# Kernel tuning notes

Measured on AMD Instinct MI355X. Metric: run time of the kernel, lower is better.

The kernel has to match this reference:

```python
import jax, jax.numpy as jnp
import numpy as np

B, N, K = 16, 2048, 32
DT = 0.01      # leapfrog step size
EPS = 1e-8     # SPD regularization (matches spd_exponential_map default)


def _sym(M):
    return 0.5 * (M + jnp.swapaxes(M, -1, -2))


def _ensure_spd(S, eps=1e-6):
    # Project to SPD cone via eigenvalue clipping: V max(L, eps) V^T
    I = jnp.eye(S.shape[-1], dtype=S.dtype)
    S = _sym(S + eps * I)
    w, v = jnp.linalg.eigh(S)
    w = jnp.clip(w, eps)
    return _sym(jnp.einsum('...ik,...k,...jk->...ij', v, w, v))


def _spd_expmap(Sigma, V, eps=1e-8):
    # exp_Sigma(V) = S^{1/2} exp(S^{-1/2} V S^{-1/2}) S^{1/2}
    I = jnp.eye(Sigma.shape[-1], dtype=Sigma.dtype)
    S = _sym(Sigma) + eps * I
    w, v = jnp.linalg.eigh(S)
    w = jnp.clip(w, eps)
    sq = jnp.sqrt(w)
    S_sqrt = jnp.einsum('...ik,...k,...jk->...ij', v, sq, v)
    S_isqrt = jnp.einsum('...ik,...k,...jk->...ij', v, 1.0 / sq, v)
    W = _sym(S_isqrt @ V @ S_isqrt)
    ww, wv = jnp.linalg.eigh(W)
    ww = jnp.clip(ww, -20.0, 20.0)
    expW = jnp.einsum('...ik,...k,...jk->...ij', wv, jnp.exp(ww), wv)
    return _ensure_spd(S_sqrt @ expW @ S_sqrt, eps)


def _retract_mod2pi(phi, margin=0.01):
    # Wrap axis-angle field into principal ball ||phi|| < pi - margin
    eps = 1e-12
    r_max = jnp.pi - margin
    theta = jnp.linalg.norm(phi, axis=-1, keepdims=True)
    theta_safe = jnp.maximum(theta, eps)
    axis = phi / theta_safe
    two_pi = 2.0 * jnp.pi
    tw = jnp.remainder(theta, two_pi)
    flip = tw > jnp.pi
    t_final = jnp.where(flip, two_pi - tw, tw)
    a_final = jnp.where(flip, -axis, axis)
    t_final = jnp.minimum(t_final, r_max)
    return a_final * t_final


def setup_inputs() -> dict:
    key = jax.random.key(0)
    k1, k2, k3, k4 = jax.random.split(key, 4)
    # Build well-conditioned SPD covariances: Wishart/K + I
    A = jax.random.normal(k1, (B, N, K, K), jnp.float32)
    Sigma = A @ jnp.swapaxes(A, -1, -2) / K + jnp.eye(K, dtype=jnp.float32)
    pi_Sigma = _sym(jax.random.normal(k2, (B, N, K, K), jnp.float32)) * 0.1
    phi = jax.random.normal(k3, (B, N, 3), jnp.float32) * 2.0
    pi_phi = jax.random.normal(k4, (B, N, 3), jnp.float32)
    return {"Sigma": Sigma, "pi_Sigma": pi_Sigma, "phi": phi, "pi_phi": pi_phi}


def reference(Sigma, pi_Sigma, phi, pi_phi):
    # One leapfrog step on the (Sigma, phi) sector of the phase space.
    # Momentum half-step: force from curved geometry dT/dSigma = 2 pi S pi
    grad_T = _sym(2.0 * (pi_Sigma @ Sigma @ pi_Sigma))
    pi_half = pi_Sigma - 0.5 * DT * grad_T
    # Position update via SPD exponential map with Sigma_dot = 2 S pi S
    Sigma_dot = 2.0 * (Sigma @ pi_half @ Sigma)
    Sigma_new = _spd_expmap(Sigma, DT * Sigma_dot, EPS)
    # Gauge field update + mod2pi retraction to principal ball
    phi_new = _retract_mod2pi(phi + DT * pi_phi)
    b, n = Sigma_new.shape[:2]
    return jnp.concatenate([Sigma_new.reshape(b, n, K * K), phi_new], axis=-1)
```

## Files before the change

### kernel.cpp

```cpp
#include <hip/hip_runtime.h>
#include <hip/hip_bf16.h>
#include <math.h>


typedef unsigned int u32;
typedef __attribute__((ext_vector_type(8))) short bf16x8;
typedef __attribute__((ext_vector_type(16))) float f32x16;

#define FPAD 33

union U4 { u32 u[4]; bf16x8 v; };

__device__ __forceinline__ bf16x8 mk8(u32 a, u32 b, u32 c, u32 d) {
    U4 t; t.u[0] = a; t.u[1] = b; t.u[2] = c; t.u[3] = d; return t.v;
}

__device__ __forceinline__ u32 pk2(float x, float y) {
    float2 f2; f2.x = x; f2.y = y;
    __hip_bfloat162 h2 = __float22bfloat162_rn(f2);
    union { __hip_bfloat162 h; u32 u; } c; c.h = h2; return c.u;
}

__device__ __forceinline__ float asfloat(u32 b) {
    union { u32 u; float f; } c; c.u = b; return c.f;
}

__device__ __forceinline__ f32x16 zero16() {
    f32x16 z;
#pragma unroll
    for (int i = 0; i < 16; ++i) z[i] = 0.f;
    return z;
}

struct Frag8 { u32 r[8]; };

__device__ __forceinline__ void swap32(u32& x, u32& y) {
    asm("v_permlane32_swap_b32 %0, %1" : "+v"(x), "+v"(y));
}

__device__ __forceinline__ void xchg(const u32* p, Frag8& B) {
    { u32 x = p[0], y = p[2]; swap32(x, y); B.r[0] = x; B.r[2] = y; }
    { u32 x = p[1], y = p[3]; swap32(x, y); B.r[1] = x; B.r[3] = y; }
    { u32 x = p[4], y = p[6]; swap32(x, y); B.r[4] = x; B.r[6] = y; }
    { u32 x = p[5], y = p[7]; swap32(x, y); B.r[5] = x; B.r[7] = y; }
}

__device__ __forceinline__ void bconv(const f32x16& X, Frag8& B) {
    u32 p[8];
#pragma unroll
    for (int i = 0; i < 8; ++i) p[i] = pk2(X[2*i], X[2*i+1]);
    xchg(p, B);
}

__device__ __forceinline__ void bconv_s(const f32x16& X, float scale, Frag8& B) {
    u32 p[8];
#pragma unroll
    for (int i = 0; i < 8; ++i) p[i] = pk2(X[2*i] * scale, X[2*i+1] * scale);
    xchg(p, B);
}

__device__ __forceinline__ void bconv_split(const f32x16& X, Frag8& Bh, Frag8& Bl) {
    u32 p[8], q[8];
#pragma unroll
    for (int i = 0; i < 8; ++i) {
        const float x = X[2*i], y = X[2*i+1];
        p[i] = pk2(x, y);
        const float lx = x - asfloat(p[i] << 16);
        const float ly = y - asfloat(p[i] & 0xffff0000u);
        q[i] = pk2(lx, ly);
    }
    xchg(p, Bh);
    xchg(q, Bl);
}

__device__ __forceinline__ f32x16 MFMA1(const u32* a, const u32* b, f32x16 acc) {
    return __builtin_amdgcn_mfma_f32_32x32x16_bf16(
        mk8(a[0], a[1], a[2], a[3]), mk8(b[0], b[1], b[2], b[3]), acc, 0, 0, 0);
}

__device__ __forceinline__ f32x16 matmul(const Frag8& A, const Frag8& B, f32x16 acc) {
    __builtin_amdgcn_s_setprio(1);
    acc = MFMA1(A.r,     B.r,     acc);
    acc = MFMA1(A.r + 4, B.r + 4, acc);
    __builtin_amdgcn_s_setprio(0);
    return acc;
}

__global__ __launch_bounds__(256)
void leapfrog_fused(const float* __restrict__ Sg, const float* __restrict__ Pg,
                    const float* __restrict__ phig, const float* __restrict__ piphig,
                    float* __restrict__ out, int total)
{
    __shared__ __align__(16) float symb[4 * 32 * FPAD];

    const int w  = threadIdx.x >> 6;
    const int l  = threadIdx.x & 63;
    const int bn = blockIdx.x * 4 + w;
    if (bn >= total) return;

    float* sy = symb + w * 32 * FPAD;

    const int fr = l & 31;
    const int h  = l >> 5;
    const size_t gbase = (size_t)bn * 1024;

    const float* Srow = Sg + gbase + fr * 32 + h * 8;
    const float* Prow = Pg + gbase + fr * 32 + h * 8;
    const float4 sv[4] = { *(const float4*)(Srow +  0), *(const float4*)(Srow +  4),
                           *(const float4*)(Srow + 16), *(const float4*)(Srow + 20) };
    const float4 pv[4] = { *(const float4*)(Prow +  0), *(const float4*)(Prow +  4),
                           *(const float4*)(Prow + 16), *(const float4*)(Prow + 20) };
    const float phx = phig[3 * bn + 0], phy = phig[3 * bn + 1], phz = phig[3 * bn + 2];
    const float qhx = piphig[3 * bn + 0], qhy = piphig[3 * bn + 1], qhz = piphig[3 * bn + 2];

    Frag8 FS, FSl, FP;
#pragma unroll
    for (int i = 0; i < 4; ++i) {
        const float4 s = sv[i];
        const float4 p = pv[i];
        const u32 ha = pk2(s.x, s.y);
        const u32 hb = pk2(s.z, s.w);
        FS.r[2*i]   = ha;
        FS.r[2*i+1] = hb;
        const float lx = s.x - asfloat(ha << 16);
        const float ly = s.y - asfloat(ha & 0xffff0000u);
        const float lz = s.z - asfloat(hb << 16);
        const float lw = s.w - asfloat(hb & 0xffff0000u);
        FSl.r[2*i]   = pk2(lx, ly);
        FSl.r[2*i+1] = pk2(lz, lw);
        FP.r[2*i]   = pk2(p.x, p.y);
        FP.r[2*i+1] = pk2(p.z, p.w);
    }

    f32x16 If;
#pragma unroll
    for (int i = 0; i < 16; ++i)
        If[i] = (((i & 3) + 8 * (i >> 2) + 4 * h) == fr) ? 1.f : 0.f;

    f32x16 U  = matmul(FS, FP, zero16());
    f32x16 Ut = matmul(FP, FS, zero16());
    Frag8 BU;  bconv(U,  BU);
    Frag8 BUt; bconv(Ut, BUt);
    f32x16 H = matmul(BUt, BU, zero16());

    f32x16 M;
#pragma unroll
    for (int i = 0; i < 16; ++i) M[i] = 0.02f * U[i] - 2e-4f * H[i];

    Frag8 FM; bconv(M, FM);

    f32x16 X = If;
#pragma unroll
    for (int d = 3; d >= 1; --d) {
        Frag8 BX; bconv_s(X, 1.f / (float)d, BX);
        X = matmul(FM, BX, If);
    }

    Frag8 BE, BEl;
    bconv_split(X, BE, BEl);
    f32x16 Y1 = matmul(FS, BE, zero16());
    f32x16 Y2 = matmul(FSl, BE, zero16());
    Y2 = matmul(FS, BEl, Y2);

#pragma unroll
    for (int i = 0; i < 16; ++i) {
        const int r = (i & 3) + 8 * (i >> 2) + 4 * h;
        sy[r * FPAD + fr] = Y1[i] + Y2[i];
    }
    const size_t obase = (size_t)bn * 1027;
#pragma unroll
    for (int k = 0; k < 16; ++k) {
        const int idx = k * 64 + l;
        const int r = idx >> 5, c = idx & 31;
        const float a = sy[r * FPAD + c];
        const float b = sy[c * FPAD + r];
        float v = 0.5f * (a + b);
        if (r == c) v += 1e-8f;
        __builtin_nontemporal_store(v, &out[obase + idx]);
    }

    if (l == 0) {
        const double TWO_PI = 6.283185307179586476925287;
        const double PI_    = 3.141592653589793238462643;
        const double x = (double)phx + 0.01 * (double)qhx;
        const double y = (double)phy + 0.01 * (double)qhy;
        const double z = (double)phz + 0.01 * (double)qhz;
        const double theta = sqrt(x * x + y * y + z * z);
        const double ts = theta > 1e-12 ? theta : 1e-12;
        const double k2 = floor(theta * (1.0 / TWO_PI));
        const double tw = theta - k2 * TWO_PI;
        double t, sgn;
        if (tw > PI_) { t = TWO_PI - tw; sgn = -1.0; }
        else          { t = tw;          sgn = 1.0;  }
        const double rmax = PI_ - 0.01;
        if (t > rmax) t = rmax;
        const double f = sgn * t / ts;
        __builtin_nontemporal_store((float)(x * f), &out[obase + 1024]);
        __builtin_nontemporal_store((float)(y * f), &out[obase + 1025]);
        __builtin_nontemporal_store((float)(z * f), &out[obase + 1026]);
    }
}

extern "C" void kernel_launch(void* const* d_in, const int* in_sizes, int n_in,
                              void* d_out, int out_size, void* d_ws, size_t ws_size,
                              hipStream_t stream)
{
    const float* Sg     = (const float*)d_in[0];
    const float* Pg     = (const float*)d_in[1];
    const float* phig   = (const float*)d_in[2];
    const float* piphig = (const float*)d_in[3];
    float* out = (float*)d_out;

    const int total = in_sizes[0] / 1024;

    leapfrog_fused<<<(total + 3) / 4, 256, 0, stream>>>(Sg, Pg, phig, piphig, out, total);
}
```

Measured before the change: 74.83 us.

## Software-pipeline matrix loads across waves and drop LDS symmetrization

Each wave now handles several matrices in a grid-stride loop, prefetching the next matrix's inputs into registers while computing the current one. The shared-memory transpose used for symmetrization is replaced by computing both S·E and E·S with extra MFMAs and averaging in registers, storing straight to global. The priority hints are also removed. This trades extra MFMA work and register pressure for no LDS round trip and better latency hiding, but cuts the grid size by a factor of four.

Result: slower. 80.87 us (+8.1%).

```diff
diff --git a/kernel.cpp b/kernel.cpp
--- a/kernel.cpp
+++ b/kernel.cpp
@@ -7,7 +7,7 @@
 typedef __attribute__((ext_vector_type(8))) short bf16x8;
 typedef __attribute__((ext_vector_type(16))) float f32x16;
 
-#define FPAD 33
+#define ITERS 4
 
 union U4 { u32 u[4]; bf16x8 v; };
 
@@ -79,45 +79,45 @@
 }
 
 __device__ __forceinline__ f32x16 matmul(const Frag8& A, const Frag8& B, f32x16 acc) {
-    __builtin_amdgcn_s_setprio(1);
     acc = MFMA1(A.r,     B.r,     acc);
     acc = MFMA1(A.r + 4, B.r + 4, acc);
-    __builtin_amdgcn_s_setprio(0);
     return acc;
 }
 
-__global__ __launch_bounds__(256)
-void leapfrog_fused(const float* __restrict__ Sg, const float* __restrict__ Pg,
-                    const float* __restrict__ phig, const float* __restrict__ piphig,
-                    float* __restrict__ out, int total)
-{
-    __shared__ __align__(16) float symb[4 * 32 * FPAD];
-
-    const int w  = threadIdx.x >> 6;
-    const int l  = threadIdx.x & 63;
-    const int bn = blockIdx.x * 4 + w;
-    if (bn >= total) return;
-
-    float* sy = symb + w * 32 * FPAD;
-
-    const int fr = l & 31;
-    const int h  = l >> 5;
+struct InBuf {
+    float4 sv[4], pv[4];
+    float  ph[3], pq[3];
+};
+
+__device__ __forceinline__ void loadm(const float* __restrict__ Sg,
+                                      const float* __restrict__ Pg,
+                                      const float* __restrict__ phig,
+                                      const float* __restrict__ piphig,
+                                      int bn, int fr, int h, InBuf& b)
+{
     const size_t gbase = (size_t)bn * 1024;
-
     const float* Srow = Sg + gbase + fr * 32 + h * 8;
     const float* Prow = Pg + gbase + fr * 32 + h * 8;
-    const float4 sv[4] = { *(const float4*)(Srow +  0), *(const float4*)(Srow +  4),
-                           *(const float4*)(Srow + 16), *(const float4*)(Srow + 20) };
-    const float4 pv[4] = { *(const float4*)(Prow +  0), *(const float4*)(Prow +  4),
-                           *(const float4*)(Prow + 16), *(const float4*)(Prow + 20) };
-    const float phx = phig[3 * bn + 0], phy = phig[3 * bn + 1], phz = phig[3 * bn + 2];
-    const float qhx = piphig[3 * bn + 0], qhy = piphig[3 * bn + 1], qhz = piphig[3 * bn + 2];
-
+    b.sv[0] = *(const float4*)(Srow +  0);
+    b.sv[1] = *(const float4*)(Srow +  4);
+    b.sv[2] = *(const float4*)(Srow + 16);
+    b.sv[3] = *(const float4*)(Srow + 20);
+    b.pv[0] = *(const float4*)(Prow +  0);
+    b.pv[1] = *(const float4*)(Prow +  4);
+    b.pv[2] = *(const float4*)(Prow + 16);
+    b.pv[3] = *(const float4*)(Prow + 20);
+    b.ph[0] = phig[3 * bn + 0]; b.ph[1] = phig[3 * bn + 1]; b.ph[2] = phig[3 * bn + 2];
+    b.pq[0] = piphig[3 * bn + 0]; b.pq[1] = piphig[3 * bn + 1]; b.pq[2] = piphig[3 * bn + 2];
+}
+
+__device__ __forceinline__ void computem(const InBuf& b, float* __restrict__ out,
+                                         int bn, int fr, int h, int l)
+{
     Frag8 FS, FSl, FP;
 #pragma unroll
     for (int i = 0; i < 4; ++i) {
-        const float4 s = sv[i];
-        const float4 p = pv[i];
+        const float4 s = b.sv[i];
+        const float4 p = b.pv[i];
         const u32 ha = pk2(s.x, s.y);
         const u32 hb = pk2(s.z, s.w);
         FS.r[2*i]   = ha;
@@ -146,7 +146,6 @@
     f32x16 M;
 #pragma unroll
     for (int i = 0; i < 16; ++i) M[i] = 0.02f * U[i] - 2e-4f * H[i];
-
     Frag8 FM; bconv(M, FM);
 
     f32x16 X = If;
@@ -158,33 +157,29 @@
 
     Frag8 BE, BEl;
     bconv_split(X, BE, BEl);
-    f32x16 Y1 = matmul(FS, BE, zero16());
-    f32x16 Y2 = matmul(FSl, BE, zero16());
-    Y2 = matmul(FS, BEl, Y2);
-
+    f32x16 Yt = matmul(FS,  BE,  zero16());
+    Yt        = matmul(FSl, BE,  Yt);
+    Yt        = matmul(FS,  BEl, Yt);
+    f32x16 Y  = matmul(BE,  FS,  zero16());
+    Y         = matmul(BEl, FS,  Y);
+    Y         = matmul(BE,  FSl, Y);
+
+    const size_t obase = (size_t)bn * 1027;
+    float* po = out + obase + (size_t)(4 * h) * 32 + fr;
 #pragma unroll
     for (int i = 0; i < 16; ++i) {
         const int r = (i & 3) + 8 * (i >> 2) + 4 * h;
-        sy[r * FPAD + fr] = Y1[i] + Y2[i];
-    }
-    const size_t obase = (size_t)bn * 1027;
-#pragma unroll
-    for (int k = 0; k < 16; ++k) {
-        const int idx = k * 64 + l;
-        const int r = idx >> 5, c = idx & 31;
-        const float a = sy[r * FPAD + c];
-        const float b = sy[c * FPAD + r];
-        float v = 0.5f * (a + b);
-        if (r == c) v += 1e-8f;
-        __builtin_nontemporal_store(v, &out[obase + idx]);
+        float v = 0.5f * (Y[i] + Yt[i]);
+        if (r == fr) v += 1e-8f;
+        __builtin_nontemporal_store(v, po + (i & 3) * 32 + (i >> 2) * 256);
     }
 
     if (l == 0) {
         const double TWO_PI = 6.283185307179586476925287;
         const double PI_    = 3.141592653589793238462643;
-        const double x = (double)phx + 0.01 * (double)qhx;
-        const double y = (double)phy + 0.01 * (double)qhy;
-        const double z = (double)phz + 0.01 * (double)qhz;
+        const double x = (double)b.ph[0] + 0.01 * (double)b.pq[0];
+        const double y = (double)b.ph[1] + 0.01 * (double)b.pq[1];
+        const double z = (double)b.ph[2] + 0.01 * (double)b.pq[2];
         const double theta = sqrt(x * x + y * y + z * z);
         const double ts = theta > 1e-12 ? theta : 1e-12;
         const double k2 = floor(theta * (1.0 / TWO_PI));
@@ -201,6 +196,35 @@
     }
 }
 
+__global__ __launch_bounds__(256)
+void leapfrog_fused(const float* __restrict__ Sg, const float* __restrict__ Pg,
+                    const float* __restrict__ phig, const float* __restrict__ piphig,
+                    float* __restrict__ out, int total)
+{
+    const int w    = threadIdx.x >> 6;
+    const int l    = threadIdx.x & 63;
+    const int wave = blockIdx.x * 4 + w;
+    const int nw   = gridDim.x * 4;
+    const int fr   = l & 31;
+    const int h    = l >> 5;
+
+    InBuf A, B;
+
+    int bn = wave;
+    if (bn < total) loadm(Sg, Pg, phig, piphig, bn, fr, h, A);
+
+#pragma unroll
+    for (int i = 0; i < ITERS; i += 2) {
+        const int bn1 = bn + nw;
+        if (bn1 < total) loadm(Sg, Pg, phig, piphig, bn1, fr, h, B);
+        if (bn  < total) computem(A, out, bn, fr, h, l);
+        const int bn2 = bn1 + nw;
+        if (bn2 < total) loadm(Sg, Pg, phig, piphig, bn2, fr, h, A);
+        if (bn1 < total) computem(B, out, bn1, fr, h, l);
+        bn = bn2;
+    }
+}
+
 extern "C" void kernel_launch(void* const* d_in, const int* in_sizes, int n_in,
                               void* d_out, int out_size, void* d_ws, size_t ws_size,
                               hipStream_t stream)
@@ -211,7 +235,8 @@
     const float* piphig = (const float*)d_in[3];
     float* out = (float*)d_out;
 
-    const int total = in_sizes[0] / 1024;
-
-    leapfrog_fused<<<(total + 3) / 4, 256, 0, stream>>>(Sg, Pg, phig, piphig, out, total);
-}
+    const int total  = in_sizes[0] / 1024;
+    const int blocks = (total + 4 * ITERS - 1) / (4 * ITERS);
+
+    leapfrog_fused<<<blocks, 256, 0, stream>>>(Sg, Pg, phig, piphig, out, total);
+}
```

## Symmetrize via transposed MFMA products instead of LDS, truncate bf16 packing

Applied to the files above, without the earlier changes.

Removes the shared-memory transpose used for symmetrization by computing both S·E and its transpose E·S with extra MFMAs, then averaging in registers and storing directly. It also replaces round-to-nearest bf16 packing with a single byte-permute truncation and drops the s_setprio hints. This trades LDS traffic and barrier-free shared stores for three additional MFMAs per matrix. Truncating to bf16 lowers accuracy slightly, which the hi/lo split partially compensates for.

New measurement: 73.10 us. 2.3% less time.

```diff
diff --git a/kernel.cpp b/kernel.cpp
--- a/kernel.cpp
+++ b/kernel.cpp
@@ -7,18 +7,14 @@
 typedef __attribute__((ext_vector_type(8))) short bf16x8;
 typedef __attribute__((ext_vector_type(16))) float f32x16;
 
-#define FPAD 33
-
 union U4 { u32 u[4]; bf16x8 v; };
 
 __device__ __forceinline__ bf16x8 mk8(u32 a, u32 b, u32 c, u32 d) {
     U4 t; t.u[0] = a; t.u[1] = b; t.u[2] = c; t.u[3] = d; return t.v;
 }
 
-__device__ __forceinline__ u32 pk2(float x, float y) {
-    float2 f2; f2.x = x; f2.y = y;
-    __hip_bfloat162 h2 = __float22bfloat162_rn(f2);
-    union { __hip_bfloat162 h; u32 u; } c; c.h = h2; return c.u;
+__device__ __forceinline__ u32 pkt(float x, float y) {
+    return __builtin_amdgcn_perm(__float_as_uint(y), __float_as_uint(x), 0x07060302u);
 }
 
 __device__ __forceinline__ float asfloat(u32 b) {
@@ -48,14 +44,14 @@
 __device__ __forceinline__ void bconv(const f32x16& X, Frag8& B) {
     u32 p[8];
 #pragma unroll
-    for (int i = 0; i < 8; ++i) p[i] = pk2(X[2*i], X[2*i+1]);
+    for (int i = 0; i < 8; ++i) p[i] = pkt(X[2*i], X[2*i+1]);
     xchg(p, B);
 }
 
 __device__ __forceinline__ void bconv_s(const f32x16& X, float scale, Frag8& B) {
     u32 p[8];
 #pragma unroll
-    for (int i = 0; i < 8; ++i) p[i] = pk2(X[2*i] * scale, X[2*i+1] * scale);
+    for (int i = 0; i < 8; ++i) p[i] = pkt(X[2*i] * scale, X[2*i+1] * scale);
     xchg(p, B);
 }
 
@@ -64,10 +60,10 @@
 #pragma unroll
     for (int i = 0; i < 8; ++i) {
         const float x = X[2*i], y = X[2*i+1];
-        p[i] = pk2(x, y);
+        p[i] = pkt(x, y);
         const float lx = x - asfloat(p[i] << 16);
         const float ly = y - asfloat(p[i] & 0xffff0000u);
-        q[i] = pk2(lx, ly);
+        q[i] = pkt(lx, ly);
     }
     xchg(p, Bh);
     xchg(q, Bl);
@@ -79,10 +75,8 @@
 }
 
 __device__ __forceinline__ f32x16 matmul(const Frag8& A, const Frag8& B, f32x16 acc) {
-    __builtin_amdgcn_s_setprio(1);
     acc = MFMA1(A.r,     B.r,     acc);
     acc = MFMA1(A.r + 4, B.r + 4, acc);
-    __builtin_amdgcn_s_setprio(0);
     return acc;
 }
 
@@ -91,14 +85,10 @@
                     const float* __restrict__ phig, const float* __restrict__ piphig,
                     float* __restrict__ out, int total)
 {
-    __shared__ __align__(16) float symb[4 * 32 * FPAD];
-
     const int w  = threadIdx.x >> 6;
     const int l  = threadIdx.x & 63;
     const int bn = blockIdx.x * 4 + w;
     if (bn >= total) return;
-
-    float* sy = symb + w * 32 * FPAD;
 
     const int fr = l & 31;
     const int h  = l >> 5;
@@ -118,18 +108,18 @@
     for (int i = 0; i < 4; ++i) {
         const float4 s = sv[i];
         const float4 p = pv[i];
-        const u32 ha = pk2(s.x, s.y);
-        const u32 hb = pk2(s.z, s.w);
+        const u32 ha = pkt(s.x, s.y);
+        const u32 hb = pkt(s.z, s.w);
         FS.r[2*i]   = ha;
         FS.r[2*i+1] = hb;
         const float lx = s.x - asfloat(ha << 16);
         const float ly = s.y - asfloat(ha & 0xffff0000u);
         const float lz = s.z - asfloat(hb << 16);
         const float lw = s.w - asfloat(hb & 0xffff0000u);
-        FSl.r[2*i]   = pk2(lx, ly);
-        FSl.r[2*i+1] = pk2(lz, lw);
-        FP.r[2*i]   = pk2(p.x, p.y);
-        FP.r[2*i+1] = pk2(p.z, p.w);
+        FSl.r[2*i]   = pkt(lx, ly);
+        FSl.r[2*i+1] = pkt(lz, lw);
+        FP.r[2*i]   = pkt(p.x, p.y);
+        FP.r[2*i+1] = pkt(p.z, p.w);
     }
 
     f32x16 If;
@@ -146,7 +136,6 @@
     f32x16 M;
 #pragma unroll
     for (int i = 0; i < 16; ++i) M[i] = 0.02f * U[i] - 2e-4f * H[i];
-
     Frag8 FM; bconv(M, FM);
 
     f32x16 X = If;
@@ -158,25 +147,21 @@
 
     Frag8 BE, BEl;
     bconv_split(X, BE, BEl);
-    f32x16 Y1 = matmul(FS, BE, zero16());
-    f32x16 Y2 = matmul(FSl, BE, zero16());
-    Y2 = matmul(FS, BEl, Y2);
-
+    f32x16 Yt = matmul(FS,  BE,  zero16());
+    f32x16 Y  = matmul(BE,  FS,  zero16());
+    Yt        = matmul(FSl, BE,  Yt);
+    Y         = matmul(BEl, FS,  Y);
+    Yt        = matmul(FS,  BEl, Yt);
+    Y         = matmul(BE,  FSl, Y);
+
+    const size_t obase = (size_t)bn * 1027;
+    float* po = out + obase + (size_t)(4 * h) * 32 + fr;
 #pragma unroll
     for (int i = 0; i < 16; ++i) {
         const int r = (i & 3) + 8 * (i >> 2) + 4 * h;
-        sy[r * FPAD + fr] = Y1[i] + Y2[i];
-    }
-    const size_t obase = (size_t)bn * 1027;
-#pragma unroll
-    for (int k = 0; k < 16; ++k) {
-        const int idx = k * 64 + l;
-        const int r = idx >> 5, c = idx & 31;
-        const float a = sy[r * FPAD + c];
-        const float b = sy[c * FPAD + r];
-        float v = 0.5f * (a + b);
-        if (r == c) v += 1e-8f;
-        __builtin_nontemporal_store(v, &out[obase + idx]);
+        float v = 0.5f * (Y[i] + Yt[i]);
+        if (r == fr) v += 1e-8f;
+        __builtin_nontemporal_store(v, po + (i & 3) * 32 + (i >> 2) * 256);
     }
 
     if (l == 0) {
```
